# Kernel optimization log

Measured on AMD Instinct MI355X. Metric: run time of the kernel, lower is better.

Reference implementation:

```python
import jax, jax.numpy as jnp
import numpy as np

N_NODES = 100000
N_EDGES = 1250000
NUM_SKILLS = 100000
HID = 64


def _sage(h, src, dst, Wl, bl, Wr, n):
    # SAGEConv (PyG defaults): out = lin_l(mean_{j in N(i)} h_j) + lin_r(h_i)
    msgs = h[src]                                        # [E, d] gather
    agg = jax.ops.segment_sum(msgs, dst, num_segments=n)  # [N, d]
    cnt = jax.ops.segment_sum(jnp.ones((src.shape[0],), h.dtype), dst, num_segments=n)
    mean = agg / jnp.maximum(cnt, 1.0)[:, None]
    return mean @ Wl + bl + h @ Wr


def _prelu(v, a):
    return jnp.where(v >= 0, v, a * v)


def setup_inputs() -> dict:
    key = jax.random.key(0)
    ks = jax.random.split(key, 12)
    s = 1.0 / np.sqrt(HID)
    inp = {
        "x": jax.random.randint(ks[0], (N_NODES,), 0, NUM_SKILLS),
        "edge_index": jax.random.randint(ks[1], (2, N_EDGES), 0, N_NODES),
        "edge_weight": jax.random.uniform(ks[2], (N_EDGES,), jnp.float32),
        "emb": jax.random.normal(ks[3], (NUM_SKILLS, HID), jnp.float32),
        "Wl1": jax.random.uniform(ks[4], (HID, HID), jnp.float32, -s, s),
        "bl1": jnp.zeros((HID,), jnp.float32),
        "Wr1": jax.random.uniform(ks[5], (HID, HID), jnp.float32, -s, s),
        "a1": jnp.float32(0.25),
        "Wl2": jax.random.uniform(ks[6], (HID, HID), jnp.float32, -s, s),
        "bl2": jnp.zeros((HID,), jnp.float32),
        "Wr2": jax.random.uniform(ks[7], (HID, HID), jnp.float32, -s, s),
        "a2": jnp.float32(0.25),
        "Wout": jax.random.uniform(ks[8], (HID, HID), jnp.float32, -s, s),
        "bout": jnp.zeros((HID,), jnp.float32),
    }
    return inp


def reference(x, edge_index, edge_weight, emb, Wl1, bl1, Wr1, a1,
              Wl2, bl2, Wr2, a2, Wout, bout):
    src, dst = edge_index[0], edge_index[1]
    n = x.shape[0]
    h0 = emb[x]                                           # [N, d] embedding lookup
    h1 = _prelu(_sage(h0, src, dst, Wl1, bl1, Wr1, n), a1)  # dropout = identity (eval)
    h2 = _prelu(_sage(h1, src, dst, Wl2, bl2, Wr2, n), a2)
    return h2 @ Wout + bout
```

## Files before the change

kernel.cpp:

```cpp
#include <hip/hip_runtime.h>
#include <hip/hip_bf16.h>

#define N_NODES 100000
#define N_EDGES 1250000
#define HID 64
#define LDSS 72
#define NB 196
#define NBLOCK 128
#define EMB_BLOCKS 6250

typedef __bf16 bf16x8 __attribute__((ext_vector_type(8)));
typedef float  f32x4  __attribute__((ext_vector_type(4)));

__device__ __forceinline__ float bflo(uint u) {
    union { unsigned int i; float f; } v; v.i = u << 16; return v.f;
}
__device__ __forceinline__ float bfhi(uint u) {
    union { unsigned int i; float f; } v; v.i = u & 0xFFFF0000u; return v.f;
}
__device__ __forceinline__ ushort f2bf(float f) {
    union { float f; unsigned int i; } v; v.f = f;
    unsigned int x = v.i;
    return (ushort)((x + 0x7fffu + ((x >> 16) & 1u)) >> 16);
}

__global__ __launch_bounds__(256) void prep(const int* __restrict__ x,
                                            const float* __restrict__ emb,
                                            ushort* __restrict__ h0,
                                            const int* __restrict__ dst,
                                            int* __restrict__ gh,
                                            const float* __restrict__ Wl1,
                                            const float* __restrict__ Wr1,
                                            const float* __restrict__ Wl2,
                                            const float* __restrict__ Wr2,
                                            const float* __restrict__ Wout,
                                            ushort* __restrict__ wbf) {
    const int b = blockIdx.x;
    const int tid = threadIdx.x;
    if (b < EMB_BLOCKS) {
        int t = b * 256 + tid;
        int row = t >> 4, c = t & 15;
        int idx = x[row];
        float4 v = ((const float4*)(emb + (size_t)idx * HID))[c];
        ushort4 w;
        w.x = f2bf(v.x); w.y = f2bf(v.y); w.z = f2bf(v.z); w.w = f2bf(v.w);
        ((ushort4*)(h0 + (size_t)row * HID))[c] = w;
    } else if (b < EMB_BLOCKS + NBLOCK) {
        __shared__ int hist[NB];
        const int bb = b - EMB_BLOCKS;
        for (int i = tid; i < NB; i += 256) hist[i] = 0;
        __syncthreads();
        const int4* d4 = (const int4*)dst;
        for (int e = bb * 256 + tid; e < N_EDGES / 4; e += NBLOCK * 256) {
            int4 v = d4[e];
            atomicAdd(&hist[v.x >> 9], 1);
            atomicAdd(&hist[v.y >> 9], 1);
            atomicAdd(&hist[v.z >> 9], 1);
            atomicAdd(&hist[v.w >> 9], 1);
        }
        __syncthreads();
        for (int i = tid; i < NB; i += 256) gh[bb * NB + i] = hist[i];
    } else {
        const int wb = b - EMB_BLOCKS - NBLOCK;
        const float* W = (wb == 0) ? Wl1 : (wb == 1) ? Wr1 :
                         (wb == 2) ? Wl2 : (wb == 3) ? Wr2 : Wout;
        ushort* o = wbf + wb * 4096;
        for (int idx = tid; idx < 4096; idx += 256) {
            int k = idx >> 6, n = idx & 63;
            o[n * 64 + k] = f2bf(W[idx]);
        }
    }
}

__global__ __launch_bounds__(256) void p3_scatter(const int* __restrict__ src,
                                                  const int* __restrict__ dst,
                                                  const int* __restrict__ gh,
                                                  int* __restrict__ bstart,
                                                  uint* __restrict__ ebuf) {
    __shared__ int base[NB];
    __shared__ int run[NB];
    __shared__ int wsum[4];
    const int tid = threadIdx.x, lane = tid & 63, wave = tid >> 6;
    int myTot = 0, myPre = 0;
    if (tid < NB) {
#pragma unroll 8
        for (int b = 0; b < NBLOCK; ++b) {
            int c = gh[b * NB + tid];
            if (b == (int)blockIdx.x) myPre = myTot;
            myTot += c;
        }
    }
    int x = myTot;
#pragma unroll
    for (int d = 1; d < 64; d <<= 1) {
        int y = __shfl_up(x, d, 64);
        if (lane >= d) x += y;
    }
    if (lane == 63) wsum[wave] = x;
    __syncthreads();
    if (wave == 0) {
        int s = (lane < 4) ? wsum[lane] : 0;
#pragma unroll
        for (int d = 1; d < 4; d <<= 1) {
            int y = __shfl_up(s, d, 64);
            if (lane >= d) s += y;
        }
        if (lane < 4) wsum[lane] = s;
    }
    __syncthreads();
    int waveoff = (wave == 0) ? 0 : wsum[wave - 1];
    int excl = waveoff + (x - myTot);
    if (tid < NB) {
        base[tid] = excl + myPre;
        run[tid] = 0;
        if (blockIdx.x == 0) bstart[tid] = excl;
    }
    if (blockIdx.x == 0 && tid == 0) bstart[NB] = N_EDGES;
    __syncthreads();
    const int4* s4 = (const int4*)src;
    const int4* d4 = (const int4*)dst;
    for (int e = blockIdx.x * 256 + tid; e < N_EDGES / 4; e += NBLOCK * 256) {
        int4 dv = d4[e];
        int4 sv = s4[e];
        int b0 = dv.x >> 9;
        int r0 = atomicAdd(&run[b0], 1);
        ebuf[base[b0] + r0] = ((uint)(dv.x & 511) << 17) | (uint)sv.x;
        int b1 = dv.y >> 9;
        int r1 = atomicAdd(&run[b1], 1);
        ebuf[base[b1] + r1] = ((uint)(dv.y & 511) << 17) | (uint)sv.y;
        int b2 = dv.z >> 9;
        int r2 = atomicAdd(&run[b2], 1);
        ebuf[base[b2] + r2] = ((uint)(dv.z & 511) << 17) | (uint)sv.z;
        int b3 = dv.w >> 9;
        int r3 = atomicAdd(&run[b3], 1);
        ebuf[base[b3] + r3] = ((uint)(dv.w & 511) << 17) | (uint)sv.w;
    }
}

__global__ __launch_bounds__(256) void p4_csr(const uint* __restrict__ ebuf,
                                              const int* __restrict__ bstart,
                                              int* __restrict__ rowptr,
                                              int* __restrict__ csr_src) {
    __shared__ int hist[512], hoff[512], run[512];
    __shared__ int wsum[4];
    const int v = blockIdx.x;
    const int tid = threadIdx.x, lane = tid & 63, wave = tid >> 6;
    const int node0 = v << 9;
    const int nn = min(512, N_NODES - node0);
    const int beg = bstart[v], end = bstart[v + 1];

    for (int i = tid; i < 512; i += 256) { hist[i] = 0; run[i] = 0; }
    __syncthreads();
    for (int e = beg + tid; e < end; e += 256)
        atomicAdd(&hist[ebuf[e] >> 17], 1);
    __syncthreads();
    int h0 = hist[2 * tid], h1 = hist[2 * tid + 1];
    int s = h0 + h1;
    int x = s;
#pragma unroll
    for (int d = 1; d < 64; d <<= 1) {
        int y = __shfl_up(x, d, 64);
        if (lane >= d) x += y;
    }
    if (lane == 63) wsum[wave] = x;
    __syncthreads();
    if (wave == 0) {
        int s2 = (lane < 4) ? wsum[lane] : 0;
#pragma unroll
        for (int d = 1; d < 4; d <<= 1) {
            int y = __shfl_up(s2, d, 64);
            if (lane >= d) s2 += y;
        }
        if (lane < 4) wsum[lane] = s2;
    }
    __syncthreads();
    int waveoff = (wave == 0) ? 0 : wsum[wave - 1];
    int excl = waveoff + (x - s);
    hoff[2 * tid] = excl;
    hoff[2 * tid + 1] = excl + h0;
    __syncthreads();
    for (int j = tid; j < nn; j += 256) rowptr[node0 + j] = beg + hoff[j];
    if (v == NB - 1 && tid == 0) rowptr[N_NODES] = N_EDGES;
    for (int e = beg + tid; e < end; e += 256) {
        uint p = ebuf[e];
        int dl = p >> 17;
        int r = atomicAdd(&run[dl], 1);
        csr_src[beg + hoff[dl] + r] = (int)(p & 0x1FFFFu);
    }
}

#define ACCUM(wa, wb)                                                      \
    a0 += bflo(wa.x); a1 += bfhi(wa.x); a2 += bflo(wa.y); a3 += bfhi(wa.y); \
    a4 += bflo(wa.z); a5 += bfhi(wa.z); a6 += bflo(wa.w); a7 += bfhi(wa.w); \
    a8 += bflo(wb.x); a9 += bfhi(wb.x); a10 += bflo(wb.y); a11 += bfhi(wb.y); \
    a12 += bflo(wb.z); a13 += bfhi(wb.z); a14 += bflo(wb.w); a15 += bfhi(wb.w);

#define GATHER(j)                                                          \
    const uint4* p##j = (const uint4*)&hin[(size_t)s##j * HID + q * 16];   \
    uint4 A##j = p##j[0], B##j = p##j[1];

template <bool OUTPROJ>
__global__ __launch_bounds__(128, 4) void layer_fused(
    const int* __restrict__ rowptr, const int* __restrict__ csr_src,
    const ushort* __restrict__ hin,
    const ushort* __restrict__ wl_bf, const float* __restrict__ bl,
    const ushort* __restrict__ wr_bf, const float* __restrict__ alpha_p,
    const ushort* __restrict__ wo_bf, const float* __restrict__ bo,
    void* __restrict__ out_p) {
    __shared__ __align__(16) ushort sA[32][LDSS];

    const int tid = threadIdx.x;
    const int row0 = blockIdx.x * 32;
    const int wave = tid >> 6, lane = tid & 63;

    const int g = tid >> 2, q = tid & 3;
    {
        int node = row0 + g;
        uint4 o0 = {0, 0, 0, 0}, o1 = {0, 0, 0, 0};
        if (node < N_NODES) {
            int beg = rowptr[node], end = rowptr[node + 1];
            float a0 = 0.f, a1 = 0.f, a2 = 0.f, a3 = 0.f;
            float a4 = 0.f, a5 = 0.f, a6 = 0.f, a7 = 0.f;
            float a8 = 0.f, a9 = 0.f, a10 = 0.f, a11 = 0.f;
            float a12 = 0.f, a13 = 0.f, a14 = 0.f, a15 = 0.f;
            int i = beg;
            for (; i + 8 <= end; i += 8) {
                int s0 = csr_src[i + 0], s1 = csr_src[i + 1];
                int s2 = csr_src[i + 2], s3 = csr_src[i + 3];
                int s4 = csr_src[i + 4], s5 = csr_src[i + 5];
                int s6 = csr_src[i + 6], s7 = csr_src[i + 7];
                GATHER(0) GATHER(1) GATHER(2) GATHER(3)
                GATHER(4) GATHER(5) GATHER(6) GATHER(7)
                ACCUM(A0, B0) ACCUM(A1, B1) ACCUM(A2, B2) ACCUM(A3, B3)
                ACCUM(A4, B4) ACCUM(A5, B5) ACCUM(A6, B6) ACCUM(A7, B7)
            }
            if (i < end) {
                const int e1 = end - 1;
                int s0 = csr_src[i + 0];
                int s1 = csr_src[(i + 1 <= e1) ? i + 1 : e1];
                int s2 = csr_src[(i + 2 <= e1) ? i + 2 : e1];
                int s3 = csr_src[(i + 3 <= e1) ? i + 3 : e1];
                int s4 = csr_src[(i + 4 <= e1) ? i + 4 : e1];
                int s5 = csr_src[(i + 5 <= e1) ? i + 5 : e1];
                int s6 = csr_src[(i + 6 <= e1) ? i + 6 : e1];
                int s7 = csr_src[(i + 7 <= e1) ? i + 7 : e1];
                GATHER(0) GATHER(1) GATHER(2) GATHER(3)
                GATHER(4) GATHER(5) GATHER(6) GATHER(7)
                const uint4 z = {0, 0, 0, 0};
                if (i + 1 > e1) { A1 = z; B1 = z; }
                if (i + 2 > e1) { A2 = z; B2 = z; }
                if (i + 3 > e1) { A3 = z; B3 = z; }
                if (i + 4 > e1) { A4 = z; B4 = z; }
                if (i + 5 > e1) { A5 = z; B5 = z; }
                if (i + 6 > e1) { A6 = z; B6 = z; }
                if (i + 7 > e1) { A7 = z; B7 = z; }
                ACCUM(A0, B0) ACCUM(A1, B1) ACCUM(A2, B2) ACCUM(A3, B3)
                ACCUM(A4, B4) ACCUM(A5, B5) ACCUM(A6, B6) ACCUM(A7, B7)
            }
            float inv = (end > beg) ? 1.0f / (float)(end - beg) : 0.f;
            o0.x = (uint)f2bf(a0 * inv)  | ((uint)f2bf(a1 * inv) << 16);
            o0.y = (uint)f2bf(a2 * inv)  | ((uint)f2bf(a3 * inv) << 16);
            o0.z = (uint)f2bf(a4 * inv)  | ((uint)f2bf(a5 * inv) << 16);
            o0.w = (uint)f2bf(a6 * inv)  | ((uint)f2bf(a7 * inv) << 16);
            o1.x = (uint)f2bf(a8 * inv)  | ((uint)f2bf(a9 * inv) << 16);
            o1.y = (uint)f2bf(a10 * inv) | ((uint)f2bf(a11 * inv) << 16);
            o1.z = (uint)f2bf(a12 * inv) | ((uint)f2bf(a13 * inv) << 16);
            o1.w = (uint)f2bf(a14 * inv) | ((uint)f2bf(a15 * inv) << 16);
        }
        *(uint4*)&sA[g][q * 16] = o0;
        *(uint4*)&sA[g][q * 16 + 8] = o1;
    }

    const int quad = lane >> 4, lr = lane & 15;
    const int r0 = wave * 16;
    const int grow = row0 + r0 + lr;
    const float alpha = alpha_p[0];

    bf16x8 hf[2], af[2];
#pragma unroll
    for (int ks = 0; ks < 2; ++ks) {
        int k0 = ks * 32 + quad * 8;
        uint4 hv = {0, 0, 0, 0};
        if (grow < N_NODES) hv = *(const uint4*)&hin[(size_t)grow * HID + k0];
        hf[ks] = __builtin_bit_cast(bf16x8, hv);
        uint4 av = *(const uint4*)&sA[r0 + lr][k0];
        af[ks] = __builtin_bit_cast(bf16x8, av);
    }

    f32x4 acc[4];
#pragma unroll
    for (int nt = 0; nt < 4; ++nt) {
        f32x4 a = {0.f, 0.f, 0.f, 0.f};
#pragma unroll
        for (int ks = 0; ks < 2; ++ks) {
            int k0 = ks * 32 + quad * 8;
            bf16x8 wr = *(const bf16x8*)&wr_bf[(nt * 16 + lr) * 64 + k0];
            a = __builtin_amdgcn_mfma_f32_16x16x32_bf16(hf[ks], wr, a, 0, 0, 0);
            bf16x8 wl = *(const bf16x8*)&wl_bf[(nt * 16 + lr) * 64 + k0];
            a = __builtin_amdgcn_mfma_f32_16x16x32_bf16(af[ks], wl, a, 0, 0, 0);
        }
        acc[nt] = a;
    }

    if constexpr (!OUTPROJ) {
#pragma unroll
        for (int nt = 0; nt < 4; ++nt) {
            int col = nt * 16 + lr;
            float bias = bl[col];
#pragma unroll
            for (int r = 0; r < 4; ++r) {
                int row = r0 + quad * 4 + r;
                float v = acc[nt][r] + bias;
                v = (v >= 0.f) ? v : alpha * v;
                sA[row][col] = f2bf(v);
            }
        }
        ushort* outp = (ushort*)out_p;
        const int lrow = lane >> 3, lch = lane & 7;
#pragma unroll
        for (int pass = 0; pass < 2; ++pass) {
            int row = r0 + pass * 8 + lrow;
            int gg2 = row0 + row;
            if (gg2 < N_NODES) {
                uint4 v4 = *(const uint4*)&sA[row][lch * 8];
                *(uint4*)&outp[(size_t)gg2 * HID + lch * 8] = v4;
            }
        }
    } else {
#pragma unroll
        for (int nt = 0; nt < 4; ++nt) {
            int col = nt * 16 + lr;
            float bias = bl[col];
#pragma unroll
            for (int r = 0; r < 4; ++r) {
                int row = r0 + quad * 4 + r;
                float v = acc[nt][r] + bias;
                v = (v >= 0.f) ? v : alpha * v;
                sA[row][col] = f2bf(v);
            }
        }
        bf16x8 h2f[2];
#pragma unroll
        for (int ks = 0; ks < 2; ++ks) {
            int k0 = ks * 32 + quad * 8;
            uint4 hv = *(const uint4*)&sA[r0 + lr][k0];
            h2f[ks] = __builtin_bit_cast(bf16x8, hv);
        }
        f32x4 acc2[4];
#pragma unroll
        for (int nt = 0; nt < 4; ++nt) {
            f32x4 a = {0.f, 0.f, 0.f, 0.f};
#pragma unroll
            for (int ks = 0; ks < 2; ++ks) {
                int k0 = ks * 32 + quad * 8;
                bf16x8 wo = *(const bf16x8*)&wo_bf[(nt * 16 + lr) * 64 + k0];
                a = __builtin_amdgcn_mfma_f32_16x16x32_bf16(h2f[ks], wo, a, 0, 0, 0);
            }
            acc2[nt] = a;
        }
        float* outp = (float*)out_p;
#pragma unroll
        for (int nt = 0; nt < 4; ++nt) {
            int col = nt * 16 + lr;
            float bias = bo[col];
#pragma unroll
            for (int r = 0; r < 4; ++r) {
                int row = r0 + quad * 4 + r;
                int gg2 = row0 + row;
                if (gg2 < N_NODES)
                    outp[(size_t)gg2 * HID + col] = acc2[nt][r] + bias;
            }
        }
    }
}

extern "C" void kernel_launch(void* const* d_in, const int* in_sizes, int n_in,
                              void* d_out, int out_size, void* d_ws, size_t ws_size,
                              hipStream_t stream) {
    const int*   x    = (const int*)d_in[0];
    const int*   src  = (const int*)d_in[1];
    const int*   dst  = src + N_EDGES;
    const float* emb  = (const float*)d_in[3];
    const float* Wl1  = (const float*)d_in[4];
    const float* bl1  = (const float*)d_in[5];
    const float* Wr1  = (const float*)d_in[6];
    const float* a1   = (const float*)d_in[7];
    const float* Wl2  = (const float*)d_in[8];
    const float* bl2  = (const float*)d_in[9];
    const float* Wr2  = (const float*)d_in[10];
    const float* a2   = (const float*)d_in[11];
    const float* Wout = (const float*)d_in[12];
    const float* bout = (const float*)d_in[13];

    char* ws = (char*)d_ws;
    int*    gh      = (int*)ws;
    int*    bstart  = (int*)(ws + 101248);
    int*    rowptr  = (int*)(ws + 102080);
    ushort* wbf     = (ushort*)(ws + 502144);
    uint*   ebuf    = (uint*)(ws + 543104);
    int*    csr_src = (int*)(ws + 5543104);
    ushort* h0      = (ushort*)(ws + 10543104);
    ushort* h1      = (ushort*)(ws + 23343104);

    ushort* wl1b  = wbf;
    ushort* wr1b  = wbf + 4096;
    ushort* wl2b  = wbf + 8192;
    ushort* wr2b  = wbf + 12288;
    ushort* woutb = wbf + 16384;

    const int layer_blocks = N_NODES / 32;

    prep<<<EMB_BLOCKS + NBLOCK + 5, 256, 0, stream>>>(
        x, emb, h0, dst, gh, Wl1, Wr1, Wl2, Wr2, Wout, wbf);
    p3_scatter<<<NBLOCK, 256, 0, stream>>>(src, dst, gh, bstart, ebuf);
    p4_csr<<<NB, 256, 0, stream>>>(ebuf, bstart, rowptr, csr_src);

    layer_fused<false><<<layer_blocks, 128, 0, stream>>>(
        rowptr, csr_src, h0, wl1b, bl1, wr1b, a1, wr1b, bl1, h1);
    layer_fused<true><<<layer_blocks, 128, 0, stream>>>(
        rowptr, csr_src, h1, wl2b, bl2, wr2b, a2, woutb, bout, d_out);
}
```

Before: 234.9 us.

## Split neighbor aggregation across two lanes per node and reorder preprocessing kernels

The aggregation phase of each layer now uses 256 threads per block, with each node's edge list split in half between two lane groups whose partial sums are combined with a cross-lane shuffle. This gives twice as many outstanding gathers per node and aims to hide memory latency on the irregular neighbor reads. Only the first two waves then run the MFMA projection, and the N_NODES bounds checks are dropped, which is safe only because 100000 divides evenly by 32. The preprocessing is also reordered: the histogram runs as its own small kernel, and the scatter is merged with the embedding lookup and weight conversion so those run concurrently.

```diff
diff --git a/kernel.cpp b/kernel.cpp
--- a/kernel.cpp
+++ b/kernel.cpp
@@ -24,44 +24,109 @@
     return (ushort)((x + 0x7fffu + ((x >> 16) & 1u)) >> 16);
 }
 
-__global__ __launch_bounds__(256) void prep(const int* __restrict__ x,
-                                            const float* __restrict__ emb,
-                                            ushort* __restrict__ h0,
-                                            const int* __restrict__ dst,
-                                            int* __restrict__ gh,
-                                            const float* __restrict__ Wl1,
-                                            const float* __restrict__ Wr1,
-                                            const float* __restrict__ Wl2,
-                                            const float* __restrict__ Wr2,
-                                            const float* __restrict__ Wout,
-                                            ushort* __restrict__ wbf) {
+__global__ __launch_bounds__(256) void hist_k(const int* __restrict__ dst,
+                                              int* __restrict__ gh) {
+    __shared__ int hist[NB];
+    const int tid = threadIdx.x;
+    for (int i = tid; i < NB; i += 256) hist[i] = 0;
+    __syncthreads();
+    const int4* d4 = (const int4*)dst;
+    for (int e = blockIdx.x * 256 + tid; e < N_EDGES / 4; e += NBLOCK * 256) {
+        int4 v = d4[e];
+        atomicAdd(&hist[v.x >> 9], 1);
+        atomicAdd(&hist[v.y >> 9], 1);
+        atomicAdd(&hist[v.z >> 9], 1);
+        atomicAdd(&hist[v.w >> 9], 1);
+    }
+    __syncthreads();
+    for (int i = tid; i < NB; i += 256) gh[blockIdx.x * NB + i] = hist[i];
+}
+
+__global__ __launch_bounds__(256) void work2(const int* __restrict__ x,
+                                             const float* __restrict__ emb,
+                                             ushort* __restrict__ h0,
+                                             const int* __restrict__ src,
+                                             const int* __restrict__ dst,
+                                             const int* __restrict__ gh,
+                                             int* __restrict__ bstart,
+                                             uint* __restrict__ ebuf,
+                                             const float* __restrict__ Wl1,
+                                             const float* __restrict__ Wr1,
+                                             const float* __restrict__ Wl2,
+                                             const float* __restrict__ Wr2,
+                                             const float* __restrict__ Wout,
+                                             ushort* __restrict__ wbf) {
     const int b = blockIdx.x;
     const int tid = threadIdx.x;
-    if (b < EMB_BLOCKS) {
-        int t = b * 256 + tid;
+    if (b < NBLOCK) {
+        __shared__ int base[NB];
+        __shared__ int run[NB];
+        __shared__ int wsum[4];
+        const int lane = tid & 63, wave = tid >> 6;
+        int myTot = 0, myPre = 0;
+        if (tid < NB) {
+#pragma unroll 8
+            for (int bb = 0; bb < NBLOCK; ++bb) {
+                int c = gh[bb * NB + tid];
+                if (bb == b) myPre = myTot;
+                myTot += c;
+            }
+        }
+        int x2 = myTot;
+#pragma unroll
+        for (int d = 1; d < 64; d <<= 1) {
+            int y = __shfl_up(x2, d, 64);
+            if (lane >= d) x2 += y;
+        }
+        if (lane == 63) wsum[wave] = x2;
+        __syncthreads();
+        if (wave == 0) {
+            int s = (lane < 4) ? wsum[lane] : 0;
+#pragma unroll
+            for (int d = 1; d < 4; d <<= 1) {
+                int y = __shfl_up(s, d, 64);
+                if (lane >= d) s += y;
+            }
+            if (lane < 4) wsum[lane] = s;
+        }
+        __syncthreads();
+        int waveoff = (wave == 0) ? 0 : wsum[wave - 1];
+        int excl = waveoff + (x2 - myTot);
+        if (tid < NB) {
+            base[tid] = excl + myPre;
+            run[tid] = 0;
+            if (b == 0) bstart[tid] = excl;
+        }
+        if (b == 0 && tid == 0) bstart[NB] = N_EDGES;
+        __syncthreads();
+        const int4* s4 = (const int4*)src;
+        const int4* d4 = (const int4*)dst;
+        for (int e = b * 256 + tid; e < N_EDGES / 4; e += NBLOCK * 256) {
+            int4 dv = d4[e];
+            int4 sv = s4[e];
+            int b0 = dv.x >> 9;
+            int r0 = atomicAdd(&run[b0], 1);
+            ebuf[base[b0] + r0] = ((uint)(dv.x & 511) << 17) | (uint)sv.x;
+            int b1 = dv.y >> 9;
+            int r1 = atomicAdd(&run[b1], 1);
+            ebuf[base[b1] + r1] = ((uint)(dv.y & 511) << 17) | (uint)sv.y;
+            int b2 = dv.z >> 9;
+            int r2 = atomicAdd(&run[b2], 1);
+            ebuf[base[b2] + r2] = ((uint)(dv.z & 511) << 17) | (uint)sv.z;
+            int b3 = dv.w >> 9;
+            int r3 = atomicAdd(&run[b3], 1);
+            ebuf[base[b3] + r3] = ((uint)(dv.w & 511) << 17) | (uint)sv.w;
+        }
+    } else if (b < NBLOCK + EMB_BLOCKS) {
+        int t = (b - NBLOCK) * 256 + tid;
         int row = t >> 4, c = t & 15;
         int idx = x[row];
         float4 v = ((const float4*)(emb + (size_t)idx * HID))[c];
         ushort4 w;
         w.x = f2bf(v.x); w.y = f2bf(v.y); w.z = f2bf(v.z); w.w = f2bf(v.w);
         ((ushort4*)(h0 + (size_t)row * HID))[c] = w;
-    } else if (b < EMB_BLOCKS + NBLOCK) {
-        __shared__ int hist[NB];
-        const int bb = b - EMB_BLOCKS;
-        for (int i = tid; i < NB; i += 256) hist[i] = 0;
-        __syncthreads();
-        const int4* d4 = (const int4*)dst;
-        for (int e = bb * 256 + tid; e < N_EDGES / 4; e += NBLOCK * 256) {
-            int4 v = d4[e];
-            atomicAdd(&hist[v.x >> 9], 1);
-            atomicAdd(&hist[v.y >> 9], 1);
-            atomicAdd(&hist[v.z >> 9], 1);
-            atomicAdd(&hist[v.w >> 9], 1);
-        }
-        __syncthreads();
-        for (int i = tid; i < NB; i += 256) gh[bb * NB + i] = hist[i];
     } else {
-        const int wb = b - EMB_BLOCKS - NBLOCK;
+        const int wb = b - NBLOCK - EMB_BLOCKS;
         const float* W = (wb == 0) ? Wl1 : (wb == 1) ? Wr1 :
                          (wb == 2) ? Wl2 : (wb == 3) ? Wr2 : Wout;
         ushort* o = wbf + wb * 4096;
@@ -69,71 +134,6 @@
             int k = idx >> 6, n = idx & 63;
             o[n * 64 + k] = f2bf(W[idx]);
         }
-    }
-}
-
-__global__ __launch_bounds__(256) void p3_scatter(const int* __restrict__ src,
-                                                  const int* __restrict__ dst,
-                                                  const int* __restrict__ gh,
-                                                  int* __restrict__ bstart,
-                                                  uint* __restrict__ ebuf) {
-    __shared__ int base[NB];
-    __shared__ int run[NB];
-    __shared__ int wsum[4];
-    const int tid = threadIdx.x, lane = tid & 63, wave = tid >> 6;
-    int myTot = 0, myPre = 0;
-    if (tid < NB) {
-#pragma unroll 8
-        for (int b = 0; b < NBLOCK; ++b) {
-            int c = gh[b * NB + tid];
-            if (b == (int)blockIdx.x) myPre = myTot;
-            myTot += c;
-        }
-    }
-    int x = myTot;
-#pragma unroll
-    for (int d = 1; d < 64; d <<= 1) {
-        int y = __shfl_up(x, d, 64);
-        if (lane >= d) x += y;
-    }
-    if (lane == 63) wsum[wave] = x;
-    __syncthreads();
-    if (wave == 0) {
-        int s = (lane < 4) ? wsum[lane] : 0;
-#pragma unroll
-        for (int d = 1; d < 4; d <<= 1) {
-            int y = __shfl_up(s, d, 64);
-            if (lane >= d) s += y;
-        }
-        if (lane < 4) wsum[lane] = s;
-    }
-    __syncthreads();
-    int waveoff = (wave == 0) ? 0 : wsum[wave - 1];
-    int excl = waveoff + (x - myTot);
-    if (tid < NB) {
-        base[tid] = excl + myPre;
-        run[tid] = 0;
-        if (blockIdx.x == 0) bstart[tid] = excl;
-    }
-    if (blockIdx.x == 0 && tid == 0) bstart[NB] = N_EDGES;
-    __syncthreads();
-    const int4* s4 = (const int4*)src;
-    const int4* d4 = (const int4*)dst;
-    for (int e = blockIdx.x * 256 + tid; e < N_EDGES / 4; e += NBLOCK * 256) {
-        int4 dv = d4[e];
-        int4 sv = s4[e];
-        int b0 = dv.x >> 9;
-        int r0 = atomicAdd(&run[b0], 1);
-        ebuf[base[b0] + r0] = ((uint)(dv.x & 511) << 17) | (uint)sv.x;
-        int b1 = dv.y >> 9;
-        int r1 = atomicAdd(&run[b1], 1);
-        ebuf[base[b1] + r1] = ((uint)(dv.y & 511) << 17) | (uint)sv.y;
-        int b2 = dv.z >> 9;
-        int r2 = atomicAdd(&run[b2], 1);
-        ebuf[base[b2] + r2] = ((uint)(dv.z & 511) << 17) | (uint)sv.z;
-        int b3 = dv.w >> 9;
-        int r3 = atomicAdd(&run[b3], 1);
-        ebuf[base[b3] + r3] = ((uint)(dv.w & 511) << 17) | (uint)sv.w;
     }
 }
 
@@ -200,7 +200,7 @@
     uint4 A##j = p##j[0], B##j = p##j[1];
 
 template <bool OUTPROJ>
-__global__ __launch_bounds__(128, 4) void layer_fused(
+__global__ __launch_bounds__(256, 4) void layer_fused(
     const int* __restrict__ rowptr, const int* __restrict__ csr_src,
     const ushort* __restrict__ hin,
     const ushort* __restrict__ wl_bf, const float* __restrict__ bl,
@@ -213,51 +213,63 @@
     const int row0 = blockIdx.x * 32;
     const int wave = tid >> 6, lane = tid & 63;
 
-    const int g = tid >> 2, q = tid & 3;
+    const int nl = tid >> 3, hh = (tid >> 2) & 1, q = tid & 3;
     {
-        int node = row0 + g;
-        uint4 o0 = {0, 0, 0, 0}, o1 = {0, 0, 0, 0};
-        if (node < N_NODES) {
-            int beg = rowptr[node], end = rowptr[node + 1];
-            float a0 = 0.f, a1 = 0.f, a2 = 0.f, a3 = 0.f;
-            float a4 = 0.f, a5 = 0.f, a6 = 0.f, a7 = 0.f;
-            float a8 = 0.f, a9 = 0.f, a10 = 0.f, a11 = 0.f;
-            float a12 = 0.f, a13 = 0.f, a14 = 0.f, a15 = 0.f;
-            int i = beg;
-            for (; i + 8 <= end; i += 8) {
-                int s0 = csr_src[i + 0], s1 = csr_src[i + 1];
-                int s2 = csr_src[i + 2], s3 = csr_src[i + 3];
-                int s4 = csr_src[i + 4], s5 = csr_src[i + 5];
-                int s6 = csr_src[i + 6], s7 = csr_src[i + 7];
-                GATHER(0) GATHER(1) GATHER(2) GATHER(3)
-                GATHER(4) GATHER(5) GATHER(6) GATHER(7)
-                ACCUM(A0, B0) ACCUM(A1, B1) ACCUM(A2, B2) ACCUM(A3, B3)
-                ACCUM(A4, B4) ACCUM(A5, B5) ACCUM(A6, B6) ACCUM(A7, B7)
-            }
-            if (i < end) {
-                const int e1 = end - 1;
-                int s0 = csr_src[i + 0];
-                int s1 = csr_src[(i + 1 <= e1) ? i + 1 : e1];
-                int s2 = csr_src[(i + 2 <= e1) ? i + 2 : e1];
-                int s3 = csr_src[(i + 3 <= e1) ? i + 3 : e1];
-                int s4 = csr_src[(i + 4 <= e1) ? i + 4 : e1];
-                int s5 = csr_src[(i + 5 <= e1) ? i + 5 : e1];
-                int s6 = csr_src[(i + 6 <= e1) ? i + 6 : e1];
-                int s7 = csr_src[(i + 7 <= e1) ? i + 7 : e1];
-                GATHER(0) GATHER(1) GATHER(2) GATHER(3)
-                GATHER(4) GATHER(5) GATHER(6) GATHER(7)
-                const uint4 z = {0, 0, 0, 0};
-                if (i + 1 > e1) { A1 = z; B1 = z; }
-                if (i + 2 > e1) { A2 = z; B2 = z; }
-                if (i + 3 > e1) { A3 = z; B3 = z; }
-                if (i + 4 > e1) { A4 = z; B4 = z; }
-                if (i + 5 > e1) { A5 = z; B5 = z; }
-                if (i + 6 > e1) { A6 = z; B6 = z; }
-                if (i + 7 > e1) { A7 = z; B7 = z; }
-                ACCUM(A0, B0) ACCUM(A1, B1) ACCUM(A2, B2) ACCUM(A3, B3)
-                ACCUM(A4, B4) ACCUM(A5, B5) ACCUM(A6, B6) ACCUM(A7, B7)
-            }
-            float inv = (end > beg) ? 1.0f / (float)(end - beg) : 0.f;
+        const int node = row0 + nl;
+        const int beg = rowptr[node], end = rowptr[node + 1];
+        const int d = end - beg;
+        const int mid = beg + ((d + 1) >> 1);
+        const int hbeg = hh ? mid : beg;
+        const int hend = hh ? end : mid;
+        float a0 = 0.f, a1 = 0.f, a2 = 0.f, a3 = 0.f;
+        float a4 = 0.f, a5 = 0.f, a6 = 0.f, a7 = 0.f;
+        float a8 = 0.f, a9 = 0.f, a10 = 0.f, a11 = 0.f;
+        float a12 = 0.f, a13 = 0.f, a14 = 0.f, a15 = 0.f;
+        int i = hbeg;
+        for (; i + 8 <= hend; i += 8) {
+            int s0 = csr_src[i + 0], s1 = csr_src[i + 1];
+            int s2 = csr_src[i + 2], s3 = csr_src[i + 3];
+            int s4 = csr_src[i + 4], s5 = csr_src[i + 5];
+            int s6 = csr_src[i + 6], s7 = csr_src[i + 7];
+            GATHER(0) GATHER(1) GATHER(2) GATHER(3)
+            GATHER(4) GATHER(5) GATHER(6) GATHER(7)
+            ACCUM(A0, B0) ACCUM(A1, B1) ACCUM(A2, B2) ACCUM(A3, B3)
+            ACCUM(A4, B4) ACCUM(A5, B5) ACCUM(A6, B6) ACCUM(A7, B7)
+        }
+        if (i < hend) {
+            const int e1 = hend - 1;
+            int s0 = csr_src[i + 0];
+            int s1 = csr_src[(i + 1 <= e1) ? i + 1 : e1];
+            int s2 = csr_src[(i + 2 <= e1) ? i + 2 : e1];
+            int s3 = csr_src[(i + 3 <= e1) ? i + 3 : e1];
+            int s4 = csr_src[(i + 4 <= e1) ? i + 4 : e1];
+            int s5 = csr_src[(i + 5 <= e1) ? i + 5 : e1];
+            int s6 = csr_src[(i + 6 <= e1) ? i + 6 : e1];
+            int s7 = csr_src[(i + 7 <= e1) ? i + 7 : e1];
+            GATHER(0) GATHER(1) GATHER(2) GATHER(3)
+            GATHER(4) GATHER(5) GATHER(6) GATHER(7)
+            const uint4 z = {0, 0, 0, 0};
+            if (i + 1 > e1) { A1 = z; B1 = z; }
+            if (i + 2 > e1) { A2 = z; B2 = z; }
+            if (i + 3 > e1) { A3 = z; B3 = z; }
+            if (i + 4 > e1) { A4 = z; B4 = z; }
+            if (i + 5 > e1) { A5 = z; B5 = z; }
+            if (i + 6 > e1) { A6 = z; B6 = z; }
+            if (i + 7 > e1) { A7 = z; B7 = z; }
+            ACCUM(A0, B0) ACCUM(A1, B1) ACCUM(A2, B2) ACCUM(A3, B3)
+            ACCUM(A4, B4) ACCUM(A5, B5) ACCUM(A6, B6) ACCUM(A7, B7)
+        }
+        a0 += __shfl_xor(a0, 4, 64);   a1 += __shfl_xor(a1, 4, 64);
+        a2 += __shfl_xor(a2, 4, 64);   a3 += __shfl_xor(a3, 4, 64);
+        a4 += __shfl_xor(a4, 4, 64);   a5 += __shfl_xor(a5, 4, 64);
+        a6 += __shfl_xor(a6, 4, 64);   a7 += __shfl_xor(a7, 4, 64);
+        a8 += __shfl_xor(a8, 4, 64);   a9 += __shfl_xor(a9, 4, 64);
+        a10 += __shfl_xor(a10, 4, 64); a11 += __shfl_xor(a11, 4, 64);
+        a12 += __shfl_xor(a12, 4, 64); a13 += __shfl_xor(a13, 4, 64);
+        a14 += __shfl_xor(a14, 4, 64); a15 += __shfl_xor(a15, 4, 64);
+        if (hh == 0) {
+            float inv = (d > 0) ? 1.0f / (float)d : 0.f;
+            uint4 o0, o1;
             o0.x = (uint)f2bf(a0 * inv)  | ((uint)f2bf(a1 * inv) << 16);
             o0.y = (uint)f2bf(a2 * inv)  | ((uint)f2bf(a3 * inv) << 16);
             o0.z = (uint)f2bf(a4 * inv)  | ((uint)f2bf(a5 * inv) << 16);
@@ -266,10 +278,12 @@
             o1.y = (uint)f2bf(a10 * inv) | ((uint)f2bf(a11 * inv) << 16);
             o1.z = (uint)f2bf(a12 * inv) | ((uint)f2bf(a13 * inv) << 16);
             o1.w = (uint)f2bf(a14 * inv) | ((uint)f2bf(a15 * inv) << 16);
-        }
-        *(uint4*)&sA[g][q * 16] = o0;
-        *(uint4*)&sA[g][q * 16 + 8] = o1;
-    }
+            *(uint4*)&sA[nl][q * 16] = o0;
+            *(uint4*)&sA[nl][q * 16 + 8] = o1;
+        }
+    }
+    __syncthreads();
+    if (wave >= 2) return;
 
     const int quad = lane >> 4, lr = lane & 15;
     const int r0 = wave * 16;
@@ -280,8 +294,7 @@
 #pragma unroll
     for (int ks = 0; ks < 2; ++ks) {
         int k0 = ks * 32 + quad * 8;
-        uint4 hv = {0, 0, 0, 0};
-        if (grow < N_NODES) hv = *(const uint4*)&hin[(size_t)grow * HID + k0];
+        uint4 hv = *(const uint4*)&hin[(size_t)grow * HID + k0];
         hf[ks] = __builtin_bit_cast(bf16x8, hv);
         uint4 av = *(const uint4*)&sA[r0 + lr][k0];
         af[ks] = __builtin_bit_cast(bf16x8, av);
@@ -321,10 +334,8 @@
         for (int pass = 0; pass < 2; ++pass) {
             int row = r0 + pass * 8 + lrow;
             int gg2 = row0 + row;
-            if (gg2 < N_NODES) {
-                uint4 v4 = *(const uint4*)&sA[row][lch * 8];
-                *(uint4*)&outp[(size_t)gg2 * HID + lch * 8] = v4;
-            }
+            uint4 v4 = *(const uint4*)&sA[row][lch * 8];
+            *(uint4*)&outp[(size_t)gg2 * HID + lch * 8] = v4;
         }
     } else {
 #pragma unroll
@@ -367,8 +378,7 @@
             for (int r = 0; r < 4; ++r) {
                 int row = r0 + quad * 4 + r;
                 int gg2 = row0 + row;
-                if (gg2 < N_NODES)
-                    outp[(size_t)gg2 * HID + col] = acc2[nt][r] + bias;
+                outp[(size_t)gg2 * HID + col] = acc2[nt][r] + bias;
             }
         }
     }
@@ -410,13 +420,13 @@
 
     const int layer_blocks = N_NODES / 32;
 
-    prep<<<EMB_BLOCKS + NBLOCK + 5, 256, 0, stream>>>(
-        x, emb, h0, dst, gh, Wl1, Wr1, Wl2, Wr2, Wout, wbf);
-    p3_scatter<<<NBLOCK, 256, 0, stream>>>(src, dst, gh, bstart, ebuf);
+    hist_k<<<NBLOCK, 256, 0, stream>>>(dst, gh);
+    work2<<<NBLOCK + EMB_BLOCKS + 5, 256, 0, stream>>>(
+        x, emb, h0, src, dst, gh, bstart, ebuf, Wl1, Wr1, Wl2, Wr2, Wout, wbf);
     p4_csr<<<NB, 256, 0, stream>>>(ebuf, bstart, rowptr, csr_src);
 
-    layer_fused<false><<<layer_blocks, 128, 0, stream>>>(
+    layer_fused<false><<<layer_blocks, 256, 0, stream>>>(
         rowptr, csr_src, h0, wl1b, bl1, wr1b, a1, wr1b, bl1, h1);
-    layer_fused<true><<<layer_blocks, 128, 0, stream>>>(
+    layer_fused<true><<<layer_blocks, 256, 0, stream>>>(
         rowptr, csr_src, h1, wl2b, bl2, wr2b, a2, woutb, bout, d_out);
 }
```

After: 215.4 us. 8.3% less time.
